# Optimization experiments

Hardware: AMD Instinct MI355X
Metric: run time of the kernel (lower is better)

Reference implementation:

```python
import jax, jax.numpy as jnp
import numpy as np

B, T, D, H = 2, 2048, 1024, 16
HD = D // H

def setup_inputs() -> dict:
    key = jax.random.key(0)
    ks = jax.random.split(key, 6)
    x = jax.random.normal(ks[0], (B, T, D), dtype=jnp.float32)
    periods = jax.random.randint(ks[1], (B, H), 0, 16, dtype=jnp.int64)
    w_qkv = jax.random.normal(ks[2], (D, 3 * D), dtype=jnp.float32) * 0.02
    b_qkv = jnp.zeros((3 * D,), dtype=jnp.float32)
    w_out = jax.random.normal(ks[3], (D, D), dtype=jnp.float32) * 0.02
    b_out = jnp.zeros((D,), dtype=jnp.float32)
    return {"x": x, "periods": periods, "w_qkv": w_qkv, "b_qkv": b_qkv,
            "w_out": w_out, "b_out": b_out}

def reference(x, periods, w_qkv, b_qkv, w_out, b_out):
    b, t, d = x.shape
    h = periods.shape[1]
    hd = d // h
    qkv = x @ w_qkv + b_qkv                     # (B,T,3D)
    qkv = qkv.reshape(b, t, 3, h, hd).transpose(2, 0, 3, 1, 4)
    q, k, v = qkv[0], qkv[1], qkv[2]            # each (B,H,T,hd)
    # periodic + causal mask, fully vectorized over (B,H)
    p = jnp.maximum(periods, 1).astype(jnp.int32)[:, :, None, None]  # (B,H,1,1)
    i = jnp.arange(t, dtype=jnp.int32)[:, None]
    j = jnp.arange(t, dtype=jnp.int32)[None, :]
    causal = (j <= i)[None, None]                                    # (1,1,T,T)
    periodic = jnp.mod((i - j)[None, None], p) == 0                  # (B,H,T,T)
    valid = causal & periodic
    scores = jnp.einsum('bhqd,bhkd->bhqk', q, k) / jnp.sqrt(jnp.float32(hd))
    scores = jnp.where(valid, scores, -jnp.inf)  # diagonal always valid -> no NaN rows
    attn = jax.nn.softmax(scores, axis=-1)
    out = jnp.einsum('bhqk,bhkd->bhqd', attn, v)
    out = out.transpose(0, 2, 1, 3).reshape(b, t, d)
    return out @ w_out + b_out
```

## Files before the change

kernel.cpp:

```cpp
#include <hip/hip_runtime.h>
#include <math.h>

#define B_  2
#define T_  2048
#define D_  1024
#define H_  16
#define HD_ 64
#define VTS (T_ + 64)

typedef float    f32x4  __attribute__((ext_vector_type(4)));
typedef _Float16 half8  __attribute__((ext_vector_type(8)));
typedef _Float16 half4v __attribute__((ext_vector_type(4)));

#define GLOAD_LDS16(g, l)                                                     \
    __builtin_amdgcn_global_load_lds(                                         \
        (__attribute__((address_space(1))) void*)(g),                         \
        (__attribute__((address_space(3))) void*)(l), 16, 0, 0)

__device__ __forceinline__ void transpose_tile(
    const float* __restrict__ in, _Float16* __restrict__ out,
    int R, int C, int r0, int c0, int tid)
{
    __shared__ float tile[32][33];
    const int tx = tid & 31, ty = tid >> 5;
    #pragma unroll
    for (int q = 0; q < 4; ++q)
        tile[ty + 8 * q][tx] = in[(size_t)(r0 + ty + 8 * q) * C + c0 + tx];
    __syncthreads();
    #pragma unroll
    for (int q = 0; q < 4; ++q)
        out[(size_t)(c0 + ty + 8 * q) * R + r0 + tx] = (_Float16)tile[tx][ty + 8 * q];
}

__global__ __launch_bounds__(256) void prep_kernel(
    const float* __restrict__ x, _Float16* __restrict__ x16,
    const float* __restrict__ w_qkv, _Float16* __restrict__ wqkvT,
    const float* __restrict__ w_out, _Float16* __restrict__ woutT)
{
    const int bx = blockIdx.x, tid = threadIdx.x;
    if (bx < 4096) {
        const int i = (bx * 256 + tid) * 4;
        float4 v = *(const float4*)(x + i);
        half4v h;
        h[0] = (_Float16)v.x; h[1] = (_Float16)v.y;
        h[2] = (_Float16)v.z; h[3] = (_Float16)v.w;
        *(half4v*)(x16 + i) = h;
    } else if (bx < 7168) {
        const int bi = bx - 4096;
        transpose_tile(w_qkv, wqkvT, D_, 3 * D_,
                       (bi / 96) * 32, (bi % 96) * 32, tid);
    } else {
        const int bi = bx - 7168;
        transpose_tile(w_out, woutT, D_, D_,
                       (bi / 32) * 32, (bi % 32) * 32, tid);
    }
}

#define GEMM_BODY(BX, BY)                                                     \
    __shared__ __align__(16) _Float16 As[128 * 64];                           \
    __shared__ __align__(16) _Float16 Bs[128 * 64];                           \
    const int tid  = threadIdx.x;                                             \
    const int lane = tid & 63;                                                \
    const int w    = tid >> 6;                                                \
    const int wm   = (w >> 1) * 64;                                           \
    const int wn   = (w & 1) * 64;                                            \
    const int srow = lane >> 3;                                     \
    const int sseg = (lane & 7) ^ srow;               \
    const _Float16* gA = A  + (size_t)((BY) * 128 + w * 32 + srow) * K + sseg * 8; \
    const _Float16* gB = Bt + (size_t)((BX) * 128 + w * 32 + srow) * K + sseg * 8; \
    _Float16* lA = &As[(w * 32) * 64];                                        \
    _Float16* lB = &Bs[(w * 32) * 64];                                        \
    f32x4 acc[4][4];                                                          \
    _Pragma("unroll")                                                         \
    for (int i = 0; i < 4; ++i)                                               \
        _Pragma("unroll")                                                     \
        for (int j = 0; j < 4; ++j)                                           \
            _Pragma("unroll")                                                 \
            for (int rr = 0; rr < 4; ++rr) acc[i][j][rr] = 0.f;               \
    const int fr  = lane & 15;                                                \
    const int fq  = lane >> 4;                                                \
    const int fsw = fr & 7;                                                   \
    for (int k0 = 0; k0 < K; k0 += 64) {                                      \
        _Pragma("unroll")                                                     \
        for (int i = 0; i < 4; ++i) {                                         \
            GLOAD_LDS16(gA + (size_t)(i * 8) * K + k0, lA + i * 8 * 64);      \
            GLOAD_LDS16(gB + (size_t)(i * 8) * K + k0, lB + i * 8 * 64);      \
        }                                                                     \
        __syncthreads();                                                      \
        _Pragma("unroll")                                                     \
        for (int kk = 0; kk < 2; ++kk) {                                      \
            half8 af[4], bf[4];                                               \
            _Pragma("unroll")                                                 \
            for (int i = 0; i < 4; ++i)                                       \
                af[i] = *(const half8*)&As[(wm + i * 16 + fr) * 64 +          \
                                           ((kk * 4 + fq) ^ fsw) * 8];        \
            _Pragma("unroll")                                                 \
            for (int j = 0; j < 4; ++j)                                       \
                bf[j] = *(const half8*)&Bs[(wn + j * 16 + fr) * 64 +          \
                                           ((kk * 4 + fq) ^ fsw) * 8];        \
            _Pragma("unroll")                                                 \
            for (int i = 0; i < 4; ++i)                                       \
                _Pragma("unroll")                                             \
                for (int j = 0; j < 4; ++j)                                   \
                    acc[i][j] = __builtin_amdgcn_mfma_f32_16x16x32_f16(       \
                        af[i], bf[j], acc[i][j], 0, 0, 0);                    \
        }                                                                     \
        __syncthreads();                                                      \
    }

__global__ __launch_bounds__(256, 4) void gemm_bt_f16_qkv(
    const _Float16* __restrict__ A, const _Float16* __restrict__ Bt,
    const float* __restrict__ bias, _Float16* __restrict__ C,
    int M, int N, int K)
{
    const int fid  = blockIdx.x;
    const int wgid = (fid & 7) * 96 + (fid >> 3);
    const int bx   = wgid % 24;
    const int by   = wgid / 24;
    GEMM_BODY(bx, by)
    #pragma unroll
    for (int j = 0; j < 4; ++j) {
        const int col = bx * 128 + wn + j * 16 + fr;
        const float bv = bias[col];
        const int which = col >> 10;
        const int hh    = (col >> 6) & 15;
        const int e     = col & 63;
        #pragma unroll
        for (int i = 0; i < 4; ++i) {
            const int row = by * 128 + wm + i * 16 + fq * 4;
            #pragma unroll
            for (int rr = 0; rr < 4; ++rr) {
                const int rowr = row + rr;
                const int b2 = rowr >> 11, t = rowr & 2047;
                const size_t dst =
                    (((size_t)(b2 * 16 + hh) * 3 + which) * 2048 + t) * 64 + e;
                C[dst] = (_Float16)(acc[i][j][rr] + bv);
            }
        }
    }
}

__global__ __launch_bounds__(256, 4) void gemm_out_128x64(
    const _Float16* __restrict__ A, const _Float16* __restrict__ Bt,
    const float* __restrict__ bias, float* __restrict__ C,
    int M, int N, int K)
{
    __shared__ __align__(16) _Float16 As[128 * 64];
    __shared__ __align__(16) _Float16 Bs[64 * 64];
    const int fid  = blockIdx.x;
    const int wgid = (fid & 7) * 64 + (fid >> 3);
    const int bx   = wgid & 15;
    const int by   = wgid >> 4;
    const int tid  = threadIdx.x;
    const int lane = tid & 63;
    const int w    = tid >> 6;
    const int srow = lane >> 3;
    const int sseg = (lane & 7) ^ srow;
    const _Float16* gA = A  + (size_t)(by * 128 + w * 32 + srow) * K + sseg * 8;
    const _Float16* gB = Bt + (size_t)(bx * 64  + w * 16 + srow) * K + sseg * 8;
    _Float16* lA = &As[(w * 32) * 64];
    _Float16* lB = &Bs[(w * 16) * 64];
    f32x4 acc[2][4];
    #pragma unroll
    for (int i = 0; i < 2; ++i)
        #pragma unroll
        for (int j = 0; j < 4; ++j)
            #pragma unroll
            for (int rr = 0; rr < 4; ++rr) acc[i][j][rr] = 0.f;
    const int fr  = lane & 15;
    const int fq  = lane >> 4;
    const int fsw = fr & 7;
    for (int k0 = 0; k0 < K; k0 += 64) {
        #pragma unroll
        for (int i = 0; i < 4; ++i)
            GLOAD_LDS16(gA + (size_t)(i * 8) * K + k0, lA + i * 8 * 64);
        #pragma unroll
        for (int i = 0; i < 2; ++i)
            GLOAD_LDS16(gB + (size_t)(i * 8) * K + k0, lB + i * 8 * 64);
        __syncthreads();
        #pragma unroll
        for (int kk = 0; kk < 2; ++kk) {
            half8 af[2], bf[4];
            #pragma unroll
            for (int i = 0; i < 2; ++i)
                af[i] = *(const half8*)&As[(w * 32 + i * 16 + fr) * 64 +
                                           ((kk * 4 + fq) ^ fsw) * 8];
            #pragma unroll
            for (int j = 0; j < 4; ++j)
                bf[j] = *(const half8*)&Bs[(j * 16 + fr) * 64 +
                                           ((kk * 4 + fq) ^ fsw) * 8];
            #pragma unroll
            for (int i = 0; i < 2; ++i)
                #pragma unroll
                for (int j = 0; j < 4; ++j)
                    acc[i][j] = __builtin_amdgcn_mfma_f32_16x16x32_f16(
                        af[i], bf[j], acc[i][j], 0, 0, 0);
        }
        __syncthreads();
    }
    #pragma unroll
    for (int j = 0; j < 4; ++j) {
        const int col = bx * 64 + j * 16 + fr;
        const float bv = bias[col];
        #pragma unroll
        for (int i = 0; i < 2; ++i) {
            const int row = by * 128 + w * 32 + i * 16 + fq * 4;
            #pragma unroll
            for (int rr = 0; rr < 4; ++rr)
                C[(size_t)(row + rr) * N + col] = acc[i][j][rr] + bv;
        }
    }
}

__global__ __launch_bounds__(256) void vt_gather_kernel(
    const _Float16* __restrict__ qkv, const int* __restrict__ periods,
    _Float16* __restrict__ vt)
{
    __shared__ _Float16 tile[64][72];
    const int fid = blockIdx.x;
    const int s   = fid >> 3;
    const int bh  = (fid & 7) + 8 * (s >> 5);
    const int c0  = (s & 31) * 64;
    int p = periods[bh]; if (p < 1) p = 1;
    const int tid = threadIdx.x;
    const int rr = tid >> 2, seg = (tid & 3) * 16;

    const int c = c0 + rr;
    int r = 0, off = 0;
    for (; r < p - 1; ++r) {
        const int n = (T_ - 1 - r) / p + 1;
        if (c < off + n) break;
        off += n;
    }
    const int t = r + (c - off) * p;

    const size_t hs = (size_t)T_ * HD_;
    const _Float16* vrow = qkv + ((size_t)bh * 3 + 2) * hs + (size_t)t * HD_ + seg;
    *(half8*)&tile[rr][seg]     = *(const half8*)(vrow);
    *(half8*)&tile[rr][seg + 8] = *(const half8*)(vrow + 8);
    __syncthreads();

    _Float16* dst = vt + ((size_t)bh * HD_ + rr) * VTS + c0 + seg;
    half8 o0, o1;
    #pragma unroll
    for (int i = 0; i < 8; ++i) o0[i] = tile[seg + i][rr];
    #pragma unroll
    for (int i = 0; i < 8; ++i) o1[i] = tile[seg + 8 + i][rr];
    *(half8*)(dst)     = o0;
    *(half8*)(dst + 8) = o1;
}

__global__ __launch_bounds__(256, 4) void attn_mfma7_kernel(
    const _Float16* __restrict__ qkv, const _Float16* __restrict__ vt,
    const int* __restrict__ periods, _Float16* __restrict__ ao)
{
    __shared__ __align__(16) _Float16 Kt0[64 * 64], Kt1[64 * 64];
    __shared__ __align__(16) _Float16 Vt0[64 * 64], Vt1[64 * 64];
    __shared__ __align__(16) _Float16 Ps[4][16 * 64];

    const int fid = blockIdx.x;
    const int s   = fid >> 3;
    const int bh  = (fid & 7) + 8 * (s / 48);
    int tix = s % 48;

    int p = periods[bh]; if (p < 1) p = 1;

    int r = -1, q0 = 0, n_r = 0, off = 0;
    for (int rr2 = 0; rr2 < p; ++rr2) {
        const int n  = (T_ - 1 - rr2) / p + 1;
        const int nt = (n + 63) >> 6;
        if (tix < nt) { r = rr2; n_r = n; q0 = (nt - 1 - tix) << 6; break; }
        tix -= nt;
        off += n;
    }
    if (r < 0) return;
    const int qn  = min(64, n_r - q0);
    const int kts = (q0 + qn + 63) >> 6;

    const int tid = threadIdx.x, lane = tid & 63, w = tid >> 6;
    const int ln = lane & 15, fq = lane >> 4;
    const int lsw = ln & 7;

    const size_t hs = (size_t)T_ * HD_;
    const _Float16* qb  = qkv + (size_t)(bh * 3) * hs;
    const _Float16* kb  = qb + hs;
    const _Float16* vtb = vt + (size_t)bh * HD_ * VTS + off;

    const int Lrow = lane >> 3;
    const int Lseg = (lane & 7) ^ Lrow;

    half8 aq0, aq1;
    {
        const int qi = min(q0 + w * 16 + ln, n_r - 1);
        const _Float16* qrow = qb + (size_t)(r + qi * p) * HD_;
        aq0 = *(const half8*)(qrow + fq * 8);
        aq1 = *(const half8*)(qrow + 32 + fq * 8);
        #pragma unroll
        for (int i2 = 0; i2 < 8; ++i2) {
            aq0[i2] = aq0[i2] * (_Float16)0.125f;
            aq1[i2] = aq1[i2] * (_Float16)0.125f;
        }
    }

    f32x4 Od[4];
    float lp[4];
    #pragma unroll
    for (int nt = 0; nt < 4; ++nt)
        #pragma unroll
        for (int rr = 0; rr < 4; ++rr) Od[nt][rr] = 0.f;
    #pragma unroll
    for (int rr = 0; rr < 4; ++rr) lp[rr] = 0.f;

#define STAGE_KV(ktn, KT, VT) do {                                            \
        const int k0n = (ktn) << 6;                                           \
        _Pragma("unroll")                                                     \
        for (int i = 0; i < 2; ++i) {                                         \
            const int rowl = w * 16 + i * 8 + Lrow;                           \
            const int kj   = min(k0n + rowl, n_r - 1);                        \
            GLOAD_LDS16(kb + (size_t)(r + kj * p) * HD_ + Lseg * 8,           \
                        &KT[(w * 16 + i * 8) * 64]);                          \
            GLOAD_LDS16(vtb + (size_t)rowl * VTS + k0n + Lseg * 8,            \
                        &VT[(w * 16 + i * 8) * 64]);                          \
        }                                                                     \
    } while (0)

#define ATTN_ITER(kt, KT, VT, KTN, VTN) do {                                  \
        const int k0 = (kt) << 6;                                             \
        if ((kt) + 1 < kts) STAGE_KV((kt) + 1, KTN, VTN);                     \
        half8 bk0[4], bk1[4];                                                 \
        _Pragma("unroll")                                                     \
        for (int nt = 0; nt < 4; ++nt) {                                      \
            const int row = nt * 16 + ln;                                     \
            bk0[nt] = *(const half8*)&KT[row * 64 + ((fq ^ lsw) << 3)];       \
            bk1[nt] = *(const half8*)&KT[row * 64 + (((4 + fq) ^ lsw) << 3)]; \
        }                                                                     \
        f32x4 Sd[4];                                                          \
        __builtin_amdgcn_s_setprio(1);                                        \
        _Pragma("unroll")                                                     \
        for (int nt = 0; nt < 4; ++nt) {                                      \
            _Pragma("unroll")                                                 \
            for (int rr = 0; rr < 4; ++rr) Sd[nt][rr] = 0.f;                  \
            Sd[nt] = __builtin_amdgcn_mfma_f32_16x16x32_f16(aq0, bk0[nt], Sd[nt], 0, 0, 0); \
            Sd[nt] = __builtin_amdgcn_mfma_f32_16x16x32_f16(aq1, bk1[nt], Sd[nt], 0, 0, 0); \
        }                                                                     \
        __builtin_amdgcn_s_setprio(0);                                        \
        const bool diag = (k0 + 64 > q0);                                     \
        _Pragma("unroll")                                                     \
        for (int rr = 0; rr < 4; ++rr) {                                      \
            const int q_abs = q0 + w * 16 + fq * 4 + rr;                      \
            float s0 = Sd[0][rr], s1 = Sd[1][rr];                             \
            float s2 = Sd[2][rr], s3 = Sd[3][rr];                             \
            if (diag) {                                                       \
                if (k0 +  0 + ln > q_abs) s0 = -INFINITY;                     \
                if (k0 + 16 + ln > q_abs) s1 = -INFINITY;                     \
                if (k0 + 32 + ln > q_abs) s2 = -INFINITY;                     \
                if (k0 + 48 + ln > q_abs) s3 = -INFINITY;                     \
            }                                                                 \
            const float e0 = __expf(s0), e1 = __expf(s1);                     \
            const float e2 = __expf(s2), e3 = __expf(s3);                     \
            lp[rr] += (e0 + e1) + (e2 + e3);                                  \
            const int prow = fq * 4 + rr, rsw = prow & 7;                     \
            _Float16* pb = &Ps[w][prow * 64] + (ln & 7);                      \
            pb[(((ln >> 3) + 0) ^ rsw) << 3] = (_Float16)e0;                  \
            pb[(((ln >> 3) + 2) ^ rsw) << 3] = (_Float16)e1;                  \
            pb[(((ln >> 3) + 4) ^ rsw) << 3] = (_Float16)e2;                  \
            pb[(((ln >> 3) + 6) ^ rsw) << 3] = (_Float16)e3;                  \
        }                                                                     \
        half8 ap0 = *(const half8*)&Ps[w][ln * 64 + ((fq ^ lsw) << 3)];       \
        half8 ap1 = *(const half8*)&Ps[w][ln * 64 + (((4 + fq) ^ lsw) << 3)]; \
        __builtin_amdgcn_s_setprio(1);                                        \
        _Pragma("unroll")                                                     \
        for (int nt = 0; nt < 4; ++nt) {                                      \
            const int row = nt * 16 + ln;                                     \
            half8 bv0 = *(const half8*)&VT[row * 64 + ((fq ^ lsw) << 3)];     \
            half8 bv1 = *(const half8*)&VT[row * 64 + (((4 + fq) ^ lsw) << 3)]; \
            Od[nt] = __builtin_amdgcn_mfma_f32_16x16x32_f16(ap0, bv0, Od[nt], 0, 0, 0); \
            Od[nt] = __builtin_amdgcn_mfma_f32_16x16x32_f16(ap1, bv1, Od[nt], 0, 0, 0); \
        }                                                                     \
        __builtin_amdgcn_s_setprio(0);                                        \
        __syncthreads();                                                      \
    } while (0)

    STAGE_KV(0, Kt0, Vt0);
    __syncthreads();

    for (int kt = 0; kt < kts; kt += 2) {
        ATTN_ITER(kt, Kt0, Vt0, Kt1, Vt1);
        if (kt + 1 < kts)
            ATTN_ITER(kt + 1, Kt1, Vt1, Kt0, Vt0);
    }

    const int bb = bh >> 4, hh = bh & 15;
    #pragma unroll
    for (int rr = 0; rr < 4; ++rr) {
        float l = lp[rr];
        l += __shfl_xor(l, 1);
        l += __shfl_xor(l, 2);
        l += __shfl_xor(l, 4);
        l += __shfl_xor(l, 8);
        const int qq = w * 16 + fq * 4 + rr;
        if (q0 + qq < n_r) {
            const int t = r + (q0 + qq) * p;
            const float inv = 1.f / l;
            _Float16* orow = ao + ((size_t)bb * T_ + t) * D_ + hh * HD_;
            #pragma unroll
            for (int nt = 0; nt < 4; ++nt)
                orow[nt * 16 + ln] = (_Float16)(Od[nt][rr] * inv);
        }
    }
#undef STAGE_KV
#undef ATTN_ITER
}

extern "C" void kernel_launch(void* const* d_in, const int* in_sizes, int n_in,
                              void* d_out, int out_size, void* d_ws, size_t ws_size,
                              hipStream_t stream)
{
    const float* x       = (const float*)d_in[0];
    const int*   periods = (const int*)  d_in[1];
    const float* w_qkv   = (const float*)d_in[2];
    const float* b_qkv   = (const float*)d_in[3];
    const float* w_out   = (const float*)d_in[4];
    const float* b_out   = (const float*)d_in[5];
    float*       out     = (float*)d_out;

    const int M = B_ * T_;

    _Float16* x16   = (_Float16*)d_ws;
    _Float16* wqkvT = x16   + (size_t)M * D_;
    _Float16* qkv16 = wqkvT + (size_t)(3 * D_) * D_;
    _Float16* ao16  = qkv16 + (size_t)M * 3 * D_;
    _Float16* woutT = ao16  + (size_t)M * D_;
    _Float16* vt16  = woutT + (size_t)D_ * D_;

    prep_kernel<<<8192, 256, 0, stream>>>(x, x16, w_qkv, wqkvT, w_out, woutT);

    gemm_bt_f16_qkv<<<768, 256, 0, stream>>>(
        x16, wqkvT, b_qkv, qkv16, M, 3 * D_, D_);

    vt_gather_kernel<<<1024, 256, 0, stream>>>(qkv16, periods, vt16);

    attn_mfma7_kernel<<<1536, 256, 0, stream>>>(qkv16, vt16, periods, ao16);

    gemm_out_128x64<<<512, 256, 0, stream>>>(
        ao16, woutT, b_out, out, M, D_, D_);
}
```

Before: 170.1 us.

## Fuse all five stages into one persistent cooperative kernel with grid syncs

Replaces the five separate launches (prep, QKV GEMM, V gather, attention, output GEMM) with one cooperative persistent kernel. Each stage loops over its work units with a grid-stride loop, shares one static shared-memory buffer, and ends with a grid-wide barrier. The aim is to remove per-launch overhead and inter-kernel gaps. In exchange, occupancy is capped to a co-resident grid, shared memory is sized for the largest stage, the block-to-work mapping changes, and every stage pays for grid synchronization.

```diff
diff --git a/kernel.cpp b/kernel.cpp
--- a/kernel.cpp
+++ b/kernel.cpp
@@ -1,5 +1,8 @@
 #include <hip/hip_runtime.h>
+#include <hip/hip_cooperative_groups.h>
 #include <math.h>
+
+namespace cg = cooperative_groups;
 
 #define B_  2
 #define T_  2048
@@ -17,11 +20,12 @@
         (__attribute__((address_space(1))) void*)(g),                         \
         (__attribute__((address_space(3))) void*)(l), 16, 0, 0)
 
-__device__ __forceinline__ void transpose_tile(
-    const float* __restrict__ in, _Float16* __restrict__ out,
-    int R, int C, int r0, int c0, int tid)
-{
-    __shared__ float tile[32][33];
+
+__device__ __forceinline__ void transpose_unit(
+    unsigned char* smemraw, const float* __restrict__ in,
+    _Float16* __restrict__ out, int R, int C, int r0, int c0, int tid)
+{
+    float (*tile)[33] = (float (*)[33])smemraw;
     const int tx = tid & 31, ty = tid >> 5;
     #pragma unroll
     for (int q = 0; q < 4; ++q)
@@ -30,14 +34,16 @@
     #pragma unroll
     for (int q = 0; q < 4; ++q)
         out[(size_t)(c0 + ty + 8 * q) * R + r0 + tx] = (_Float16)tile[tx][ty + 8 * q];
-}
-
-__global__ __launch_bounds__(256) void prep_kernel(
+    __syncthreads();
+}
+
+__device__ __forceinline__ void prep_unit(
+    int bx, unsigned char* smem,
     const float* __restrict__ x, _Float16* __restrict__ x16,
     const float* __restrict__ w_qkv, _Float16* __restrict__ wqkvT,
     const float* __restrict__ w_out, _Float16* __restrict__ woutT)
 {
-    const int bx = blockIdx.x, tid = threadIdx.x;
+    const int tid = threadIdx.x;
     if (bx < 4096) {
         const int i = (bx * 256 + tid) * 4;
         float4 v = *(const float4*)(x + i);
@@ -47,18 +53,16 @@
         *(half4v*)(x16 + i) = h;
     } else if (bx < 7168) {
         const int bi = bx - 4096;
-        transpose_tile(w_qkv, wqkvT, D_, 3 * D_,
+        transpose_unit(smem, w_qkv, wqkvT, D_, 3 * D_,
                        (bi / 96) * 32, (bi % 96) * 32, tid);
     } else {
         const int bi = bx - 7168;
-        transpose_tile(w_out, woutT, D_, D_,
+        transpose_unit(smem, w_out, woutT, D_, D_,
                        (bi / 32) * 32, (bi % 32) * 32, tid);
     }
 }
 
-#define GEMM_BODY(BX, BY)                                                     \
-    __shared__ __align__(16) _Float16 As[128 * 64];                           \
-    __shared__ __align__(16) _Float16 Bs[128 * 64];                           \
+#define GEMM_BODY_P(BX, BY)                                                   \
     const int tid  = threadIdx.x;                                             \
     const int lane = tid & 63;                                                \
     const int w    = tid >> 6;                                                \
@@ -108,16 +112,17 @@
         __syncthreads();                                                      \
     }
 
-__global__ __launch_bounds__(256, 4) void gemm_bt_f16_qkv(
+__device__ __forceinline__ void qkv_unit(
+    int v, unsigned char* smem,
     const _Float16* __restrict__ A, const _Float16* __restrict__ Bt,
-    const float* __restrict__ bias, _Float16* __restrict__ C,
-    int M, int N, int K)
-{
-    const int fid  = blockIdx.x;
-    const int wgid = (fid & 7) * 96 + (fid >> 3);
+    const float* __restrict__ bias, _Float16* __restrict__ C, int M, int N, int K)
+{
+    _Float16* As = (_Float16*)smem;
+    _Float16* Bs = (_Float16*)(smem + 16384);
+    const int wgid = (v & 7) * 96 + (v >> 3);
     const int bx   = wgid % 24;
     const int by   = wgid / 24;
-    GEMM_BODY(bx, by)
+    GEMM_BODY_P(bx, by)
     #pragma unroll
     for (int j = 0; j < 4; ++j) {
         const int col = bx * 128 + wn + j * 16 + fr;
@@ -140,15 +145,14 @@
     }
 }
 
-__global__ __launch_bounds__(256, 4) void gemm_out_128x64(
+__device__ __forceinline__ void out_unit(
+    int v, unsigned char* smem,
     const _Float16* __restrict__ A, const _Float16* __restrict__ Bt,
-    const float* __restrict__ bias, float* __restrict__ C,
-    int M, int N, int K)
-{
-    __shared__ __align__(16) _Float16 As[128 * 64];
-    __shared__ __align__(16) _Float16 Bs[64 * 64];
-    const int fid  = blockIdx.x;
-    const int wgid = (fid & 7) * 64 + (fid >> 3);
+    const float* __restrict__ bias, float* __restrict__ C, int M, int N, int K)
+{
+    _Float16* As = (_Float16*)smem;
+    _Float16* Bs = (_Float16*)(smem + 16384);
+    const int wgid = (v & 7) * 64 + (v >> 3);
     const int bx   = wgid & 15;
     const int by   = wgid >> 4;
     const int tid  = threadIdx.x;
@@ -212,14 +216,14 @@
     }
 }
 
-__global__ __launch_bounds__(256) void vt_gather_kernel(
+__device__ __forceinline__ void vt_unit(
+    int v, unsigned char* smem,
     const _Float16* __restrict__ qkv, const int* __restrict__ periods,
     _Float16* __restrict__ vt)
 {
-    __shared__ _Float16 tile[64][72];
-    const int fid = blockIdx.x;
-    const int s   = fid >> 3;
-    const int bh  = (fid & 7) + 8 * (s >> 5);
+    _Float16 (*tile)[72] = (_Float16 (*)[72])smem;
+    const int s   = v >> 3;
+    const int bh  = (v & 7) + 8 * (s >> 5);
     const int c0  = (s & 31) * 64;
     int p = periods[bh]; if (p < 1) p = 1;
     const int tid = threadIdx.x;
@@ -248,19 +252,22 @@
     for (int i = 0; i < 8; ++i) o1[i] = tile[seg + 8 + i][rr];
     *(half8*)(dst)     = o0;
     *(half8*)(dst + 8) = o1;
-}
-
-__global__ __launch_bounds__(256, 4) void attn_mfma7_kernel(
+    __syncthreads();
+}
+
+__device__ __forceinline__ void attn_unit(
+    int v, unsigned char* smem,
     const _Float16* __restrict__ qkv, const _Float16* __restrict__ vt,
     const int* __restrict__ periods, _Float16* __restrict__ ao)
 {
-    __shared__ __align__(16) _Float16 Kt0[64 * 64], Kt1[64 * 64];
-    __shared__ __align__(16) _Float16 Vt0[64 * 64], Vt1[64 * 64];
-    __shared__ __align__(16) _Float16 Ps[4][16 * 64];
-
-    const int fid = blockIdx.x;
-    const int s   = fid >> 3;
-    const int bh  = (fid & 7) + 8 * (s / 48);
+    _Float16* Kt0 = (_Float16*)(smem);
+    _Float16* Kt1 = (_Float16*)(smem + 8192);
+    _Float16* Vt0 = (_Float16*)(smem + 16384);
+    _Float16* Vt1 = (_Float16*)(smem + 24576);
+    _Float16 (*Ps)[16 * 64] = (_Float16 (*)[16 * 64])(smem + 32768);
+
+    const int s   = v >> 3;
+    const int bh  = (v & 7) + 8 * (s / 48);
     int tix = s % 48;
 
     int p = periods[bh]; if (p < 1) p = 1;
@@ -412,6 +419,38 @@
 #undef ATTN_ITER
 }
 
+__global__ __launch_bounds__(256, 2) void fused_all(
+    const float* x, const int* periods, const float* w_qkv,
+    const float* b_qkv, const float* w_out, const float* b_out, float* out,
+    _Float16* x16, _Float16* wqkvT, _Float16* qkv16, _Float16* ao16,
+    _Float16* woutT, _Float16* vt16)
+{
+    cg::grid_group gg = cg::this_grid();
+    __shared__ __align__(16) unsigned char smem[40960];
+    const int bid = blockIdx.x;
+    const int GS  = gridDim.x;
+    const int M   = B_ * T_;
+
+    for (int v = bid; v < 8192; v += GS)
+        prep_unit(v, smem, x, x16, w_qkv, wqkvT, w_out, woutT);
+    gg.sync();
+
+    for (int v = bid; v < 768; v += GS)
+        qkv_unit(v, smem, x16, wqkvT, b_qkv, qkv16, M, 3 * D_, D_);
+    gg.sync();
+
+    for (int v = bid; v < 1024; v += GS)
+        vt_unit(v, smem, qkv16, periods, vt16);
+    gg.sync();
+
+    for (int v = bid; v < 1536; v += GS)
+        attn_unit(v, smem, qkv16, vt16, periods, ao16);
+    gg.sync();
+
+    for (int v = bid; v < 512; v += GS)
+        out_unit(v, smem, ao16, woutT, b_out, out, M, D_, D_);
+}
+
 extern "C" void kernel_launch(void* const* d_in, const int* in_sizes, int n_in,
                               void* d_out, int out_size, void* d_ws, size_t ws_size,
                               hipStream_t stream)
@@ -423,6 +462,7 @@
     const float* w_out   = (const float*)d_in[4];
     const float* b_out   = (const float*)d_in[5];
     float*       out     = (float*)d_out;
+    (void)in_sizes; (void)n_in; (void)out_size; (void)ws_size;
 
     const int M = B_ * T_;
 
@@ -433,15 +473,19 @@
     _Float16* woutT = ao16  + (size_t)M * D_;
     _Float16* vt16  = woutT + (size_t)D_ * D_;
 
-    prep_kernel<<<8192, 256, 0, stream>>>(x, x16, w_qkv, wqkvT, w_out, woutT);
-
-    gemm_bt_f16_qkv<<<768, 256, 0, stream>>>(
-        x16, wqkvT, b_qkv, qkv16, M, 3 * D_, D_);
-
-    vt_gather_kernel<<<1024, 256, 0, stream>>>(qkv16, periods, vt16);
-
-    attn_mfma7_kernel<<<1536, 256, 0, stream>>>(qkv16, vt16, periods, ao16);
-
-    gemm_out_128x64<<<512, 256, 0, stream>>>(
-        ao16, woutT, b_out, out, M, D_, D_);
-}
+    int maxb = 0;
+    hipOccupancyMaxActiveBlocksPerMultiprocessor(&maxb, fused_all, 256, 0);
+    if (maxb < 1) maxb = 1;
+    int grid = maxb * 256;
+    if (grid > 1024) grid = 1024;
+    grid &= ~7;
+    if (grid < 8) grid = 8;
+
+    void* args[] = {
+        (void*)&x, (void*)&periods, (void*)&w_qkv, (void*)&b_qkv,
+        (void*)&w_out, (void*)&b_out, (void*)&out,
+        (void*)&x16, (void*)&wqkvT, (void*)&qkv16, (void*)&ao16,
+        (void*)&woutT, (void*)&vt16
+    };
+    hipLaunchCooperativeKernel(fused_all, dim3(grid), dim3(256), args, 0, stream);
+}
```

Result: slower. 362.9 us (+113.3%).
